# Kernel tuning notes

Hardware: AMD Instinct MI355X
Metric: run time of the kernel (lower is better)

Reference implementation:

```python
import jax, jax.numpy as jnp
import numpy as np

N_RAYS = 65536
S = 192            # samples per ray (uniform segments for the reference)
N = N_RAYS * S
LAMBDA_OPACITY = 0.001
LAMBDA_DISTORTION = 0.001


def setup_inputs() -> dict:
    key = jax.random.key(0)
    ks = jax.random.split(key, 9)
    rgb_coarse = jax.random.uniform(ks[0], (N_RAYS, 3), dtype=jnp.float32)
    rgb_fine = jax.random.uniform(ks[1], (N_RAYS, 3), dtype=jnp.float32)
    rgb_target = jax.random.uniform(ks[2], (N_RAYS, 3), dtype=jnp.float32)
    depth = jax.random.uniform(ks[3], (N_RAYS,), dtype=jnp.float32)
    depth_target = jax.random.uniform(ks[4], (N_RAYS,), dtype=jnp.float32)
    opacity = jax.random.uniform(ks[5], (N_RAYS,), dtype=jnp.float32,
                                 minval=0.01, maxval=0.99)
    # sample weights roughly normalized per ray; positive intervals / midpoints
    ws = jax.random.uniform(ks[6], (N,), dtype=jnp.float32) / S
    deltas = jax.random.uniform(ks[7], (N,), dtype=jnp.float32) * 0.01
    ts = jax.random.uniform(ks[8], (N,), dtype=jnp.float32)
    ray_idx = jnp.arange(N_RAYS, dtype=jnp.int32)
    rays_a = jnp.stack([ray_idx, ray_idx * S,
                        jnp.full((N_RAYS,), S, dtype=jnp.int32)], axis=1)
    return {"rgb_coarse": rgb_coarse, "rgb_fine": rgb_fine,
            "rgb_target": rgb_target, "depth": depth,
            "depth_target": depth_target, "opacity": opacity,
            "ws": ws, "deltas": deltas, "ts": ts, "rays_a": rays_a}


def distortion_loss(ws, deltas, ts, rays_a):
    """Mip-NeRF 360 distortion loss per ray via inclusive/exclusive prefix scans.

    loss_r = sum_{i,j in r} w_i w_j |t_i - t_j| + (1/3) sum_{i in r} w_i^2 d_i
    computed as sum_i 2*w_i*(t_i*W_excl_i - (wt)_excl_i) + w_i^2 d_i / 3,
    where *_excl are within-ray exclusive prefix sums.
    """
    n_rays = rays_a.shape[0]
    starts = rays_a[:, 1]
    # segment id of each sample via its ray's start offset (starts are sorted)
    seg = jnp.searchsorted(starts, jnp.arange(ws.shape[0], dtype=starts.dtype),
                           side='right') - 1
    wts = ws * ts
    excl_w = jnp.cumsum(ws) - ws           # global exclusive prefix of w
    excl_wt = jnp.cumsum(wts) - wts        # global exclusive prefix of w*t
    # subtract prefix value at each segment's start -> within-ray exclusive scan
    w_prefix = excl_w - excl_w[starts][seg]
    wt_prefix = excl_wt - excl_wt[starts][seg]
    li = 2.0 * ws * (ts * w_prefix - wt_prefix) + ws * ws * deltas / 3.0
    loss_seg = jax.ops.segment_sum(li, seg, num_segments=n_rays)
    # place each segment's loss at its ray_idx
    return jnp.zeros(n_rays, ws.dtype).at[rays_a[:, 0]].add(loss_seg)


def reference(rgb_coarse, rgb_fine, rgb_target, depth, depth_target,
              opacity, ws, deltas, ts, rays_a):
    d_rgb = jnp.mean((rgb_coarse - rgb_target) ** 2, axis=1)
    d_rgb = d_rgb + jnp.mean((rgb_fine - rgb_target) ** 2, axis=1)
    d_depth = jnp.abs(depth - depth_target)
    o = opacity + 1e-10
    d_opacity = LAMBDA_OPACITY * (-o * jnp.log(o))
    d_distortion = LAMBDA_DISTORTION * distortion_loss(ws, deltas, ts, rays_a)
    return (d_rgb, d_depth, d_opacity, d_distortion)
```

## Files before the change

kernel.cpp:

```cpp
#include <hip/hip_runtime.h>
#include <math.h>

#define N_RAYS 65536
#define LAMBDA_OPACITY 0.001f
#define LAMBDA_DISTORTION 0.001f

template <int CTRL, int ROW_MASK>
__device__ __forceinline__ float dpp_add(float x) {
    int s = __builtin_amdgcn_update_dpp(0, __float_as_int(x),
                                        CTRL, ROW_MASK, 0xf, false);
    return x + __int_as_float(s);
}

__device__ __forceinline__ float wave64_incl_scan(float x) {
    x = dpp_add<0x111, 0xf>(x);
    x = dpp_add<0x112, 0xf>(x);
    x = dpp_add<0x114, 0xf>(x);
    x = dpp_add<0x118, 0xf>(x);
    x = dpp_add<0x142, 0xa>(x);
    x = dpp_add<0x143, 0xc>(x);
    return x;
}

__global__ __launch_bounds__(256)
void distortion_kernel(
    const float* __restrict__ ws,
    const float* __restrict__ deltas,
    const float* __restrict__ ts,
    const int*   __restrict__ rays_a,
    float* __restrict__ out)
{
    const int lane = threadIdx.x & 63;
    const int ray  = blockIdx.x * 4 + (threadIdx.x >> 6);
    if (ray >= N_RAYS) return;

    const int out_ray = rays_a[ray * 3 + 0];
    const int start   = rays_a[ray * 3 + 1];
    const int count   = rays_a[ray * 3 + 2];

    float w[4] = {0.f, 0.f, 0.f, 0.f};
    float t[4] = {0.f, 0.f, 0.f, 0.f};
    float d[4] = {0.f, 0.f, 0.f, 0.f};

    if (count == 192 && ((start & 3) == 0)) {
        if (lane < 48) {
            const float4 vw = *(const float4*)(ws     + start + 4 * lane);
            const float4 vt = *(const float4*)(ts     + start + 4 * lane);
            const float4 vd = *(const float4*)(deltas + start + 4 * lane);
            __builtin_amdgcn_sched_barrier(0);
            w[0] = vw.x; w[1] = vw.y; w[2] = vw.z; w[3] = vw.w;
            t[0] = vt.x; t[1] = vt.y; t[2] = vt.z; t[3] = vt.w;
            d[0] = vd.x; d[1] = vd.y; d[2] = vd.z; d[3] = vd.w;
        }
    } else {
        #pragma unroll
        for (int e = 0; e < 4; ++e) {
            const int p  = 4 * lane + e;
            const bool ok = p < count;
            w[e] = ok ? ws[start + p]     : 0.f;
            t[e] = ok ? ts[start + p]     : 0.f;
            d[e] = ok ? deltas[start + p] : 0.f;
        }
    }

    const float wt0 = w[0] * t[0], wt1 = w[1] * t[1];
    const float wt2 = w[2] * t[2], wt3 = w[3] * t[3];
    const float lw  = (w[0] + w[1]) + (w[2] + w[3]);
    const float lwt = (wt0 + wt1) + (wt2 + wt3);

    const float iw  = wave64_incl_scan(lw);
    const float iwt = wave64_incl_scan(lwt);

    float e_w  = iw  - lw;
    float e_wt = iwt - lwt;

    float acc = 0.f;
    #pragma unroll
    for (int e = 0; e < 4; ++e) {
        acc += 2.f * w[e] * (t[e] * e_w - e_wt) + w[e] * w[e] * d[e] * (1.f / 3.f);
        e_w  += w[e];
        e_wt += w[e] * t[e];
    }

    const float tot = wave64_incl_scan(acc);
    if (lane == 63)
        out[3 * N_RAYS + out_ray] = LAMBDA_DISTORTION * tot;
}

__global__ __launch_bounds__(256)
void perray_kernel(
    const float* __restrict__ rgb_coarse,
    const float* __restrict__ rgb_fine,
    const float* __restrict__ rgb_target,
    const float* __restrict__ depth,
    const float* __restrict__ depth_target,
    const float* __restrict__ opacity,
    float* __restrict__ out)
{
    const int r = blockIdx.x * blockDim.x + threadIdx.x;
    if (r >= N_RAYS) return;

    const float rt0 = rgb_target[r * 3 + 0];
    const float rt1 = rgb_target[r * 3 + 1];
    const float rt2 = rgb_target[r * 3 + 2];
    const float c0 = rgb_coarse[r * 3 + 0] - rt0;
    const float c1 = rgb_coarse[r * 3 + 1] - rt1;
    const float c2 = rgb_coarse[r * 3 + 2] - rt2;
    const float f0 = rgb_fine[r * 3 + 0] - rt0;
    const float f1 = rgb_fine[r * 3 + 1] - rt1;
    const float f2 = rgb_fine[r * 3 + 2] - rt2;

    out[r] = (c0 * c0 + c1 * c1 + c2 * c2) * (1.f / 3.f)
           + (f0 * f0 + f1 * f1 + f2 * f2) * (1.f / 3.f);

    out[N_RAYS + r] = fabsf(depth[r] - depth_target[r]);

    const float o = opacity[r] + 1e-10f;
    out[2 * N_RAYS + r] = LAMBDA_OPACITY * (-o * logf(o));
}

extern "C" void kernel_launch(void* const* d_in, const int* in_sizes, int n_in,
                              void* d_out, int out_size, void* d_ws, size_t ws_size,
                              hipStream_t stream) {
    const float* rgb_coarse   = (const float*)d_in[0];
    const float* rgb_fine     = (const float*)d_in[1];
    const float* rgb_target   = (const float*)d_in[2];
    const float* depth        = (const float*)d_in[3];
    const float* depth_target = (const float*)d_in[4];
    const float* opacity      = (const float*)d_in[5];
    const float* ws           = (const float*)d_in[6];
    const float* deltas       = (const float*)d_in[7];
    const float* ts           = (const float*)d_in[8];
    const int*   rays_a       = (const int*)d_in[9];
    float* out = (float*)d_out;

    distortion_kernel<<<N_RAYS / 4, 256, 0, stream>>>(
        ws, deltas, ts, rays_a, out);

    perray_kernel<<<N_RAYS / 256, 256, 0, stream>>>(
        rgb_coarse, rgb_fine, rgb_target, depth, depth_target, opacity, out);
}
```

Baseline: 179.5 us.

## Process eight rays per wave with software-pipelined prefetch of next ray

Each wave now handles eight rays instead of one. Ray metadata for the block is staged once in shared memory, and the float4 loads for the next ray are issued before the current ray's scans run, so load latency overlaps with compute. This cuts the block count eightfold and amortises the per-ray metadata loads. In exchange it uses more registers for the double-buffered loads and leaves fewer waves in flight to hide memory latency.

```diff
diff --git a/kernel.cpp b/kernel.cpp
--- a/kernel.cpp
+++ b/kernel.cpp
@@ -4,6 +4,10 @@
 #define N_RAYS 65536
 #define LAMBDA_OPACITY 0.001f
 #define LAMBDA_DISTORTION 0.001f
+
+#define WAVES_PER_BLOCK 4
+#define RAYS_PER_WAVE 8
+#define RAYS_PER_BLOCK (WAVES_PER_BLOCK * RAYS_PER_WAVE)
 
 template <int CTRL, int ROW_MASK>
 __device__ __forceinline__ float dpp_add(float x) {
@@ -30,61 +34,95 @@
     const int*   __restrict__ rays_a,
     float* __restrict__ out)
 {
+    __shared__ int smeta[RAYS_PER_BLOCK * 3];
+
     const int lane = threadIdx.x & 63;
-    const int ray  = blockIdx.x * 4 + (threadIdx.x >> 6);
-    if (ray >= N_RAYS) return;
+    const int wave = threadIdx.x >> 6;
 
-    const int out_ray = rays_a[ray * 3 + 0];
-    const int start   = rays_a[ray * 3 + 1];
-    const int count   = rays_a[ray * 3 + 2];
+    if (threadIdx.x < RAYS_PER_BLOCK * 3)
+        smeta[threadIdx.x] = rays_a[blockIdx.x * (RAYS_PER_BLOCK * 3) + threadIdx.x];
+    __syncthreads();
 
-    float w[4] = {0.f, 0.f, 0.f, 0.f};
-    float t[4] = {0.f, 0.f, 0.f, 0.f};
-    float d[4] = {0.f, 0.f, 0.f, 0.f};
+    const int m0 = wave * (RAYS_PER_WAVE * 3);
 
-    if (count == 192 && ((start & 3) == 0)) {
-        if (lane < 48) {
-            const float4 vw = *(const float4*)(ws     + start + 4 * lane);
-            const float4 vt = *(const float4*)(ts     + start + 4 * lane);
-            const float4 vd = *(const float4*)(deltas + start + 4 * lane);
+    int r_st[RAYS_PER_WAVE], r_ct[RAYS_PER_WAVE];
+    #pragma unroll
+    for (int i = 0; i < RAYS_PER_WAVE; ++i) {
+        r_st[i] = smeta[m0 + 3 * i + 1];
+        r_ct[i] = smeta[m0 + 3 * i + 2];
+    }
+
+    float4 vw, vt, vd;
+    {
+        const bool fastp = (r_ct[0] == 192) && ((r_st[0] & 3) == 0);
+        if (fastp && lane < 48) {
+            vw = *(const float4*)(ws     + r_st[0] + 4 * lane);
+            vt = *(const float4*)(ts     + r_st[0] + 4 * lane);
+            vd = *(const float4*)(deltas + r_st[0] + 4 * lane);
+        }
+        __builtin_amdgcn_sched_barrier(0);
+    }
+
+    #pragma unroll
+    for (int i = 0; i < RAYS_PER_WAVE; ++i) {
+        const bool fastp = (r_ct[i] == 192) && ((r_st[i] & 3) == 0);
+
+        float4 nw, nt, nd;
+        if (i + 1 < RAYS_PER_WAVE) {
+            const bool fastn = (r_ct[i + 1] == 192) && ((r_st[i + 1] & 3) == 0);
+            if (fastn && lane < 48) {
+                nw = *(const float4*)(ws     + r_st[i + 1] + 4 * lane);
+                nt = *(const float4*)(ts     + r_st[i + 1] + 4 * lane);
+                nd = *(const float4*)(deltas + r_st[i + 1] + 4 * lane);
+            }
             __builtin_amdgcn_sched_barrier(0);
-            w[0] = vw.x; w[1] = vw.y; w[2] = vw.z; w[3] = vw.w;
-            t[0] = vt.x; t[1] = vt.y; t[2] = vt.z; t[3] = vt.w;
-            d[0] = vd.x; d[1] = vd.y; d[2] = vd.z; d[3] = vd.w;
         }
-    } else {
+
+        float w[4] = {0.f, 0.f, 0.f, 0.f};
+        float t[4] = {0.f, 0.f, 0.f, 0.f};
+        float d[4] = {0.f, 0.f, 0.f, 0.f};
+        if (fastp) {
+            if (lane < 48) {
+                w[0]=vw.x; w[1]=vw.y; w[2]=vw.z; w[3]=vw.w;
+                t[0]=vt.x; t[1]=vt.y; t[2]=vt.z; t[3]=vt.w;
+                d[0]=vd.x; d[1]=vd.y; d[2]=vd.z; d[3]=vd.w;
+            }
+        } else {
+            #pragma unroll
+            for (int e = 0; e < 4; ++e) {
+                const int p  = 4 * lane + e;
+                const bool ok = p < r_ct[i];
+                w[e] = ok ? ws[r_st[i] + p]     : 0.f;
+                t[e] = ok ? ts[r_st[i] + p]     : 0.f;
+                d[e] = ok ? deltas[r_st[i] + p] : 0.f;
+            }
+        }
+
+        const float wt0 = w[0] * t[0], wt1 = w[1] * t[1];
+        const float wt2 = w[2] * t[2], wt3 = w[3] * t[3];
+        const float lw  = (w[0] + w[1]) + (w[2] + w[3]);
+        const float lwt = (wt0 + wt1) + (wt2 + wt3);
+
+        const float iw  = wave64_incl_scan(lw);
+        const float iwt = wave64_incl_scan(lwt);
+
+        float e_w  = iw  - lw;
+        float e_wt = iwt - lwt;
+
+        float acc = 0.f;
         #pragma unroll
         for (int e = 0; e < 4; ++e) {
-            const int p  = 4 * lane + e;
-            const bool ok = p < count;
-            w[e] = ok ? ws[start + p]     : 0.f;
-            t[e] = ok ? ts[start + p]     : 0.f;
-            d[e] = ok ? deltas[start + p] : 0.f;
+            acc += 2.f * w[e] * (t[e] * e_w - e_wt) + w[e] * w[e] * d[e] * (1.f / 3.f);
+            e_w  += w[e];
+            e_wt += w[e] * t[e];
         }
+
+        const float tot = wave64_incl_scan(acc);
+        if (lane == 63)
+            out[3 * N_RAYS + smeta[m0 + 3 * i]] = LAMBDA_DISTORTION * tot;
+
+        vw = nw; vt = nt; vd = nd;
     }
-
-    const float wt0 = w[0] * t[0], wt1 = w[1] * t[1];
-    const float wt2 = w[2] * t[2], wt3 = w[3] * t[3];
-    const float lw  = (w[0] + w[1]) + (w[2] + w[3]);
-    const float lwt = (wt0 + wt1) + (wt2 + wt3);
-
-    const float iw  = wave64_incl_scan(lw);
-    const float iwt = wave64_incl_scan(lwt);
-
-    float e_w  = iw  - lw;
-    float e_wt = iwt - lwt;
-
-    float acc = 0.f;
-    #pragma unroll
-    for (int e = 0; e < 4; ++e) {
-        acc += 2.f * w[e] * (t[e] * e_w - e_wt) + w[e] * w[e] * d[e] * (1.f / 3.f);
-        e_w  += w[e];
-        e_wt += w[e] * t[e];
-    }
-
-    const float tot = wave64_incl_scan(acc);
-    if (lane == 63)
-        out[3 * N_RAYS + out_ray] = LAMBDA_DISTORTION * tot;
 }
 
 __global__ __launch_bounds__(256)
@@ -134,7 +172,7 @@
     const int*   rays_a       = (const int*)d_in[9];
     float* out = (float*)d_out;
 
-    distortion_kernel<<<N_RAYS / 4, 256, 0, stream>>>(
+    distortion_kernel<<<N_RAYS / RAYS_PER_BLOCK, 256, 0, stream>>>(
         ws, deltas, ts, rays_a, out);
 
     perray_kernel<<<N_RAYS / 256, 256, 0, stream>>>(
```

After: 186.6 us. +3.9%, slower.

## Process 16 rays per wave with full-lane packed loads and segmented scans

Applied to the files above, without the earlier changes.

Each wave now handles 16 contiguous rays and streams their 3072 samples as 12 fully populated float4 loads per array, so no lanes sit idle as they did when 48 of 64 lanes served one 192-sample ray. Ray boundaries inside a 256-sample chunk are handled by splitting the wave scan at a fixed lane and carrying partial sums across iterations. A block-level check confirms the uniform layout (start = 192*r, count = 192) and otherwise falls back to a general per-ray loop that works for any count. The cost is more scans and shuffles per element and a block sync, and the grid is 16x smaller, which reduces parallelism.

```diff
diff --git a/kernel.cpp b/kernel.cpp
--- a/kernel.cpp
+++ b/kernel.cpp
@@ -4,6 +4,9 @@
 #define N_RAYS 65536
 #define LAMBDA_OPACITY 0.001f
 #define LAMBDA_DISTORTION 0.001f
+
+#define RAYS_PER_BLOCK 64
+#define RAYS_PER_WAVE 16
 
 template <int CTRL, int ROW_MASK>
 __device__ __forceinline__ float dpp_add(float x) {
@@ -31,60 +34,131 @@
     float* __restrict__ out)
 {
     const int lane = threadIdx.x & 63;
-    const int ray  = blockIdx.x * 4 + (threadIdx.x >> 6);
-    if (ray >= N_RAYS) return;
-
-    const int out_ray = rays_a[ray * 3 + 0];
-    const int start   = rays_a[ray * 3 + 1];
-    const int count   = rays_a[ray * 3 + 2];
-
-    float w[4] = {0.f, 0.f, 0.f, 0.f};
-    float t[4] = {0.f, 0.f, 0.f, 0.f};
-    float d[4] = {0.f, 0.f, 0.f, 0.f};
-
-    if (count == 192 && ((start & 3) == 0)) {
-        if (lane < 48) {
-            const float4 vw = *(const float4*)(ws     + start + 4 * lane);
-            const float4 vt = *(const float4*)(ts     + start + 4 * lane);
-            const float4 vd = *(const float4*)(deltas + start + 4 * lane);
-            __builtin_amdgcn_sched_barrier(0);
-            w[0] = vw.x; w[1] = vw.y; w[2] = vw.z; w[3] = vw.w;
-            t[0] = vt.x; t[1] = vt.y; t[2] = vt.z; t[3] = vt.w;
-            d[0] = vd.x; d[1] = vd.y; d[2] = vd.z; d[3] = vd.w;
+    const int wave = threadIdx.x >> 6;
+    const int rblk = blockIdx.x * RAYS_PER_BLOCK;
+
+    __shared__ int ok_s;
+    if (threadIdx.x == 0) ok_s = 1;
+    __syncthreads();
+    if (threadIdx.x < RAYS_PER_BLOCK) {
+        const int r  = rblk + threadIdx.x;
+        const int st = rays_a[3 * r + 1];
+        const int ct = rays_a[3 * r + 2];
+        if (st != 192 * r || ct != 192) ok_s = 0;
+    }
+    __syncthreads();
+    const bool ok = (ok_s != 0);
+
+    const int ray0 = rblk + wave * RAYS_PER_WAVE;
+
+    if (ok) {
+        const float4* wp4 = (const float4*)(ws     + 192 * ray0);
+        const float4* tp4 = (const float4*)(ts     + 192 * ray0);
+        const float4* dp4 = (const float4*)(deltas + 192 * ray0);
+
+        int my_or = 0;
+        if (lane < RAYS_PER_WAVE) my_or = rays_a[3 * (ray0 + lane) + 0];
+
+        float carry_w = 0.f, carry_wt = 0.f, carry_acc = 0.f;
+
+        #pragma unroll
+        for (int i = 0; i < 12; ++i) {
+            const int m    = i % 3;
+            const int B    = (m == 0) ? 48 : (m == 1) ? 32 : 16;
+            const int Lray = (4 * i) / 3;
+
+            const int q = 64 * i + lane;
+            const float4 vw = wp4[q];
+            const float4 vt = tp4[q];
+            const float4 vd = dp4[q];
+
+            const float w0 = vw.x, w1 = vw.y, w2 = vw.z, w3 = vw.w;
+            const float t0 = vt.x, t1 = vt.y, t2 = vt.z, t3 = vt.w;
+
+            const float lw  = (w0 + w1) + (w2 + w3);
+            const float lwt = (w0 * t0 + w1 * t1) + (w2 * t2 + w3 * t3);
+
+            const float Iw  = wave64_incl_scan(lw);
+            const float Iwt = wave64_incl_scan(lwt);
+
+            const float Pw  = __shfl(Iw,  B - 1);
+            const float Pwt = __shfl(Iwt, B - 1);
+
+            const bool right = (lane >= B);
+            float e_w  = (Iw  - lw ) + (right ? -Pw  : carry_w);
+            float e_wt = (Iwt - lwt) + (right ? -Pwt : carry_wt);
+
+            float acc = 0.f;
+            acc += 2.f * w0 * (t0 * e_w - e_wt) + w0 * w0 * vd.x * (1.f / 3.f);
+            e_w += w0; e_wt += w0 * t0;
+            acc += 2.f * w1 * (t1 * e_w - e_wt) + w1 * w1 * vd.y * (1.f / 3.f);
+            e_w += w1; e_wt += w1 * t1;
+            acc += 2.f * w2 * (t2 * e_w - e_wt) + w2 * w2 * vd.z * (1.f / 3.f);
+            e_w += w2; e_wt += w2 * t2;
+            acc += 2.f * w3 * (t3 * e_w - e_wt) + w3 * w3 * vd.w * (1.f / 3.f);
+
+            const float Iacc = wave64_incl_scan(acc);
+            const float Pacc = __shfl(Iacc, B - 1);
+
+            const int lor = __shfl(my_or, Lray);
+            if (lane == B - 1)
+                out[3 * N_RAYS + lor] = LAMBDA_DISTORTION * (carry_acc + Iacc);
+
+            if (m == 2) {
+                const int ror = __shfl(my_or, Lray + 1);
+                if (lane == 63)
+                    out[3 * N_RAYS + ror] = LAMBDA_DISTORTION * (Iacc - Pacc);
+                carry_w = 0.f; carry_wt = 0.f; carry_acc = 0.f;
+            } else {
+                const float Tw   = __shfl(Iw,   63);
+                const float Twt  = __shfl(Iwt,  63);
+                const float Tacc = __shfl(Iacc, 63);
+                carry_w   = Tw   - Pw;
+                carry_wt  = Twt  - Pwt;
+                carry_acc = Tacc - Pacc;
+            }
         }
     } else {
-        #pragma unroll
-        for (int e = 0; e < 4; ++e) {
-            const int p  = 4 * lane + e;
-            const bool ok = p < count;
-            w[e] = ok ? ws[start + p]     : 0.f;
-            t[e] = ok ? ts[start + p]     : 0.f;
-            d[e] = ok ? deltas[start + p] : 0.f;
+        for (int r = ray0; r < ray0 + RAYS_PER_WAVE; ++r) {
+            const int orv = rays_a[3 * r + 0];
+            const int st  = rays_a[3 * r + 1];
+            const int ct  = rays_a[3 * r + 2];
+
+            float c_w = 0.f, c_wt = 0.f, racc = 0.f;
+            for (int base = 0; base < ct; base += 256) {
+                float w[4], t[4], d[4];
+                #pragma unroll
+                for (int e = 0; e < 4; ++e) {
+                    const int p  = base + 4 * lane + e;
+                    const bool okp = p < ct;
+                    w[e] = okp ? ws[st + p]     : 0.f;
+                    t[e] = okp ? ts[st + p]     : 0.f;
+                    d[e] = okp ? deltas[st + p] : 0.f;
+                }
+                const float lw  = (w[0] + w[1]) + (w[2] + w[3]);
+                const float lwt = (w[0]*t[0] + w[1]*t[1]) + (w[2]*t[2] + w[3]*t[3]);
+                const float Iw  = wave64_incl_scan(lw);
+                const float Iwt = wave64_incl_scan(lwt);
+
+                float e_w  = c_w  + Iw  - lw;
+                float e_wt = c_wt + Iwt - lwt;
+
+                float acc = 0.f;
+                #pragma unroll
+                for (int e = 0; e < 4; ++e) {
+                    acc += 2.f * w[e] * (t[e] * e_w - e_wt) + w[e] * w[e] * d[e] * (1.f / 3.f);
+                    e_w  += w[e];
+                    e_wt += w[e] * t[e];
+                }
+                const float Iacc = wave64_incl_scan(acc);
+                racc += __shfl(Iacc, 63);
+                c_w  += __shfl(Iw,  63);
+                c_wt += __shfl(Iwt, 63);
+            }
+            if (lane == 63)
+                out[3 * N_RAYS + orv] = LAMBDA_DISTORTION * racc;
         }
     }
-
-    const float wt0 = w[0] * t[0], wt1 = w[1] * t[1];
-    const float wt2 = w[2] * t[2], wt3 = w[3] * t[3];
-    const float lw  = (w[0] + w[1]) + (w[2] + w[3]);
-    const float lwt = (wt0 + wt1) + (wt2 + wt3);
-
-    const float iw  = wave64_incl_scan(lw);
-    const float iwt = wave64_incl_scan(lwt);
-
-    float e_w  = iw  - lw;
-    float e_wt = iwt - lwt;
-
-    float acc = 0.f;
-    #pragma unroll
-    for (int e = 0; e < 4; ++e) {
-        acc += 2.f * w[e] * (t[e] * e_w - e_wt) + w[e] * w[e] * d[e] * (1.f / 3.f);
-        e_w  += w[e];
-        e_wt += w[e] * t[e];
-    }
-
-    const float tot = wave64_incl_scan(acc);
-    if (lane == 63)
-        out[3 * N_RAYS + out_ray] = LAMBDA_DISTORTION * tot;
 }
 
 __global__ __launch_bounds__(256)
@@ -134,7 +208,7 @@
     const int*   rays_a       = (const int*)d_in[9];
     float* out = (float*)d_out;
 
-    distortion_kernel<<<N_RAYS / 4, 256, 0, stream>>>(
+    distortion_kernel<<<N_RAYS / RAYS_PER_BLOCK, 256, 0, stream>>>(
         ws, deltas, ts, rays_a, out);
 
     perray_kernel<<<N_RAYS / 256, 256, 0, stream>>>(
```

Measured after the change: 184.5 us. 1.03x slower.
